# Kernel optimization log

Hardware: AMD Instinct MI355X
Metric: run time of the kernel (lower is better)

The kernel has to match this reference:

```python
import jax, jax.numpy as jnp
import numpy as np

N, E = 50000, 800000
DIN, DOUT, DEDGE, HEADS = 128, 128, 64, 1


def setup_inputs() -> dict:
    key = jax.random.key(0)
    ks = jax.random.split(key, 16)
    s = 0.02
    inp = {
        "x": jax.random.normal(ks[0], (N, DIN), jnp.float32),
        "edge_index": jax.random.randint(ks[1], (2, E), 0, N, dtype=jnp.int32),
        "edge_attr": jax.random.normal(ks[2], (E, DEDGE), jnp.float32),
        # TransformerConv params (PyG defaults: q/k/v/skip have bias, lin_edge has no bias)
        "Wq": jax.random.normal(ks[3], (DIN, HEADS * DOUT), jnp.float32) * s,
        "bq": jnp.zeros((HEADS * DOUT,), jnp.float32),
        "Wk": jax.random.normal(ks[4], (DIN, HEADS * DOUT), jnp.float32) * s,
        "bk": jnp.zeros((HEADS * DOUT,), jnp.float32),
        "Wv": jax.random.normal(ks[5], (DIN, HEADS * DOUT), jnp.float32) * s,
        "bv": jnp.zeros((HEADS * DOUT,), jnp.float32),
        "We": jax.random.normal(ks[6], (DEDGE, HEADS * DOUT), jnp.float32) * s,
        "Wskip": jax.random.normal(ks[7], (DIN, HEADS * DOUT), jnp.float32) * s,
        "bskip": jnp.zeros((HEADS * DOUT,), jnp.float32),
        # LayerNorm
        "ln_g": jnp.ones((DOUT,), jnp.float32),
        "ln_b": jnp.zeros((DOUT,), jnp.float32),
        # GatedResidualConnection
        "Wres": jax.random.normal(ks[8], (DIN, DOUT), jnp.float32) * s,
        "bres": jnp.zeros((DOUT,), jnp.float32),
        "Wgate": jax.random.normal(ks[9], (DIN, 1), jnp.float32) * s,
        "bgate": jnp.zeros((1,), jnp.float32),
    }
    return inp


def _transformer_conv(x, edge_index, edge_attr, Wq, bq, Wk, bk, Wv, bv, We, Wskip, bskip):
    H, C = HEADS, DOUT
    src, dst = edge_index[0], edge_index[1]  # j -> i (aggregate at dst)
    q = (x @ Wq + bq).reshape(-1, H, C)
    k = (x @ Wk + bk).reshape(-1, H, C)
    v = (x @ Wv + bv).reshape(-1, H, C)
    e = (edge_attr @ We).reshape(-1, H, C)  # [E,H,C]
    k_j = k[src] + e
    v_j = v[src] + e
    q_i = q[dst]
    alpha = jnp.sum(q_i * k_j, axis=-1) / jnp.sqrt(jnp.float32(C))  # [E,H]
    # segment softmax over incoming edges of each dst node
    amax = jax.ops.segment_max(alpha, dst, num_segments=N)  # [N,H]
    ex = jnp.exp(alpha - amax[dst])
    denom = jax.ops.segment_sum(ex, dst, num_segments=N)  # [N,H]
    p = ex / denom[dst]  # [E,H]
    out = jax.ops.segment_sum(p[..., None] * v_j, dst, num_segments=N)  # [N,H,C]
    out = out.reshape(-1, H * C)
    out = out + (x @ Wskip + bskip)  # root weight skip
    return out


def reference(x, edge_index, edge_attr, Wq, bq, Wk, bk, Wv, bv, We, Wskip, bskip,
              ln_g, ln_b, Wres, bres, Wgate, bgate):
    out = _transformer_conv(x, edge_index, edge_attr, Wq, bq, Wk, bk, Wv, bv, We, Wskip, bskip)
    # LayerNorm(out_channels)
    mu = jnp.mean(out, axis=-1, keepdims=True)
    var = jnp.mean(jnp.square(out - mu), axis=-1, keepdims=True)
    out = (out - mu) / jnp.sqrt(var + 1e-5) * ln_g + ln_b
    out = jax.nn.relu(out)
    # gated residual
    residual = x @ Wres + bres
    gate = jax.nn.sigmoid(x @ Wgate + bgate)  # [N,1]
    return gate * out + (1.0 - gate) * residual
```

## Files before the change

kernel.cpp:

```cpp
#include <hip/hip_runtime.h>
#include <math.h>

#define NN 50000
#define EE 800000
#define NPAD 50048
#define PC 768

typedef short bf16x8 __attribute__((ext_vector_type(8)));
typedef float f32x4 __attribute__((ext_vector_type(4)));

#define ASCALE 0.08838834764831845f

__device__ inline unsigned short f2bf(float f)
{
    unsigned u = __float_as_uint(f);
    u = u + 0x7fff + ((u >> 16) & 1);
    return (unsigned short)(u >> 16);
}

__device__ inline float bfu(unsigned short us)
{
    return __uint_as_float((unsigned)us << 16);
}

__global__ __launch_bounds__(256) void k_wprep(const float* __restrict__ Wq,
                                               const float* __restrict__ bq,
                                               const float* __restrict__ We,
                                               float* __restrict__ wqe,
                                               float* __restrict__ bqe)
{
    int idx = blockIdx.x * 256 + threadIdx.x;
    if (idx < 8192) {
        int r = idx >> 6, m = idx & 63;
        float acc = 0.f;
        for (int c = 0; c < 128; ++c) acc += Wq[r * 128 + c] * We[m * 128 + c];
        wqe[r * 64 + m] = acc;
    } else if (idx < 8256) {
        int m = idx - 8192;
        float acc = 0.f;
        for (int c = 0; c < 128; ++c) acc += bq[c] * We[m * 128 + c];
        bqe[m] = acc;
    }
}

__global__ __launch_bounds__(256) void k_packx(const float* __restrict__ x,
                                               short* __restrict__ Xb)
{
    int t = blockIdx.x * 256 + threadIdx.x;
    int base = t * 4;
    if (base >= NPAD * 128) return;
    short s0 = 0, s1 = 0, s2 = 0, s3 = 0;
    if (base < NN * 128) {
        const float4 v = *(const float4*)(x + base);
        s0 = f2bf(v.x); s1 = f2bf(v.y); s2 = f2bf(v.z); s3 = f2bf(v.w);
    }
    short4 o; o.x = s0; o.y = s1; o.z = s2; o.w = s3;
    *(short4*)(Xb + base) = o;
}

__global__ __launch_bounds__(256) void k_packw(
    const float* __restrict__ Wq, const float* __restrict__ bq,
    const float* __restrict__ Wk, const float* __restrict__ bk,
    const float* __restrict__ Wv, const float* __restrict__ bv,
    const float* __restrict__ Wskip, const float* __restrict__ bskip,
    const float* __restrict__ Wres, const float* __restrict__ bres,
    const float* __restrict__ Wgate, const float* __restrict__ bgate,
    const float* __restrict__ wqe, const float* __restrict__ bqe,
    const float* __restrict__ We,
    short* __restrict__ WT, float* __restrict__ bias,
    unsigned short* __restrict__ WeTb)
{
    int idx = blockIdx.x * 256 + threadIdx.x;
    if (idx < PC * 128) {
        int col = idx >> 7, k = idx & 127;
        float v;
        if (col < 128)      v = Wq[k * 128 + col];
        else if (col < 256) v = Wk[k * 128 + (col - 128)];
        else if (col < 384) v = Wv[k * 128 + (col - 256)];
        else if (col < 512) v = Wskip[k * 128 + (col - 384)];
        else if (col < 640) v = Wres[k * 128 + (col - 512)];
        else if (col < 704) v = wqe[k * 64 + (col - 640)];
        else if (col == 704) v = Wgate[k];
        else                v = 0.f;
        WT[col * 128 + k] = (short)f2bf(v);
    } else if (idx < PC * 128 + PC) {
        int col = idx - PC * 128;
        float b;
        if (col < 128)      b = bq[col];
        else if (col < 256) b = bk[col - 128];
        else if (col < 384) b = bv[col - 256];
        else if (col < 512) b = bskip[col - 384];
        else if (col < 640) b = bres[col - 512];
        else if (col < 704) b = bqe[col - 640];
        else if (col == 704) b = bgate[0];
        else                b = 0.f;
        bias[col] = b;
    } else if (idx < PC * 128 + PC + 128 * 72) {
        int i2 = idx - (PC * 128 + PC);
        int c = i2 / 72, kk = i2 % 72;
        WeTb[i2] = (kk < 64) ? f2bf(We[kk * 128 + c]) : (unsigned short)0;
    }
}

#define LROW 136
__global__ __launch_bounds__(256) void k_gemm(const short* __restrict__ Xb,
                                              const short* __restrict__ WT,
                                              const float* __restrict__ bias,
                                              float* __restrict__ Pq,
                                              unsigned short* __restrict__ Pe,
                                              unsigned short* __restrict__ KVb16)
{
    __shared__ short Al[128 * LROW];
    __shared__ short Bl[64 * LROW];

    int bn = blockIdx.x;
    int bm = blockIdx.y;
    int tid = threadIdx.x;

    const short* gA = Xb + (size_t)bm * 128 * 128;
    const short* gB = WT + (size_t)bn * 64 * 128;

#pragma unroll
    for (int it = 0; it < 8; ++it) {
        int g = it * 256 + tid;
        int row = g >> 4, c8 = g & 15;
        *(bf16x8*)&Al[row * LROW + c8 * 8] = *(const bf16x8*)(gA + g * 8);
    }
#pragma unroll
    for (int it = 0; it < 4; ++it) {
        int g = it * 256 + tid;
        int row = g >> 4, c8 = g & 15;
        *(bf16x8*)&Bl[row * LROW + c8 * 8] = *(const bf16x8*)(gB + g * 8);
    }
    __syncthreads();

    int wave = tid >> 6, lane = tid & 63;
    int quad = lane >> 4, l16 = lane & 15;
    int r0 = wave * 32;

    f32x4 acc[2][4] = {};
#pragma unroll
    for (int ks = 0; ks < 4; ++ks) {
        int k0 = ks * 32 + quad * 8;
        bf16x8 af0 = *(const bf16x8*)&Al[(r0 + l16) * LROW + k0];
        bf16x8 af1 = *(const bf16x8*)&Al[(r0 + 16 + l16) * LROW + k0];
#pragma unroll
        for (int cn = 0; cn < 4; ++cn) {
            bf16x8 bfr = *(const bf16x8*)&Bl[(cn * 16 + l16) * LROW + k0];
            acc[0][cn] = __builtin_amdgcn_mfma_f32_16x16x32_bf16(af0, bfr, acc[0][cn], 0, 0, 0);
            acc[1][cn] = __builtin_amdgcn_mfma_f32_16x16x32_bf16(af1, bfr, acc[1][cn], 0, 0, 0);
        }
    }

    bool isKV = (bn >= 2 && bn <= 5);
#pragma unroll
    for (int half = 0; half < 2; ++half) {
        int growb = bm * 128 + r0 + half * 16 + quad * 4;
#pragma unroll
        for (int cn = 0; cn < 4; ++cn) {
            int gcol = bn * 64 + cn * 16 + l16;
            float b = bias[gcol];
#pragma unroll
            for (int i = 0; i < 4; ++i) {
                int grow = growb + i;
                if (grow < NN) {
                    float v = acc[half][cn][i] + b;
                    if (bn < 2) {
                        Pq[(size_t)grow * 128 + gcol] = v;
                    } else if (isKV) {
                        int c, sub;
                        if (gcol < 192)      { c = gcol - 128; sub = 0; }
                        else if (gcol < 256) { c = gcol - 192; sub = 1; }
                        else if (gcol < 320) { c = gcol - 256; sub = 2; }
                        else                 { c = gcol - 320; sub = 3; }
                        KVb16[(size_t)grow * 256 + c * 4 + sub] = f2bf(v);
                    } else if (gcol <= 704) {
                        if (gcol == 704) v = 1.f / (1.f + __expf(-v));
                        Pe[(size_t)grow * 384 + (gcol - 384)] = f2bf(v);
                    }
                }
            }
        }
    }
}

__global__ __launch_bounds__(256) void k_hist(const int* __restrict__ ei,
                                              int* __restrict__ deg, int E)
{
    int e = blockIdx.x * 256 + threadIdx.x;
    if (e < E) atomicAdd(&deg[ei[E + e]], 1);
}

__global__ __launch_bounds__(256) void k_scan1(const int* __restrict__ deg,
                                               int* __restrict__ rs,
                                               int* __restrict__ cs, int n)
{
    __shared__ int sh[256];
    int base = blockIdx.x * 1024;
    int t = threadIdx.x;
    int idx = base + t * 4;
    int v[4];
#pragma unroll
    for (int k = 0; k < 4; ++k) v[k] = (idx + k < n) ? deg[idx + k] : 0;
    int sum = v[0] + v[1] + v[2] + v[3];
    sh[t] = sum;
    __syncthreads();
    for (int off = 1; off < 256; off <<= 1) {
        int add = (t >= off) ? sh[t - off] : 0;
        __syncthreads();
        sh[t] += add;
        __syncthreads();
    }
    int run = sh[t] - sum;
    if (t == 255) cs[blockIdx.x] = sh[255];
#pragma unroll
    for (int k = 0; k < 4; ++k) {
        if (idx + k < n) rs[idx + k] = run;
        run += v[k];
    }
}

__global__ void k_scan2(int* __restrict__ cs, int nc)
{
    __shared__ int sh[64];
    int t = threadIdx.x;
    sh[t] = (t < nc) ? cs[t] : 0;
    __syncthreads();
    if (t == 0) {
        int acc = 0;
        for (int i = 0; i < nc; ++i) { int v = sh[i]; sh[i] = acc; acc += v; }
    }
    __syncthreads();
    if (t < nc) cs[t] = sh[t];
}

__global__ __launch_bounds__(256) void k_scan3(int* __restrict__ rs,
                                               const int* __restrict__ cs,
                                               int* __restrict__ cur, int n, int E)
{
    int i = blockIdx.x * 256 + threadIdx.x;
    if (i < n) {
        int v = rs[i] + cs[i >> 10];
        rs[i] = v;
        cur[i] = v;
    } else if (i == n) {
        rs[n] = E;
    }
}

__global__ __launch_bounds__(256) void k_scatter(const int* __restrict__ ei,
                                                 int* __restrict__ cur,
                                                 int2* __restrict__ sj, int E)
{
    int e = blockIdx.x * 256 + threadIdx.x;
    if (e < E) {
        int d = ei[E + e];
        int pos = atomicAdd(&cur[d], 1);
        int2 v; v.x = ei[e]; v.y = e;
        sj[pos] = v;
    }
}

__global__ __launch_bounds__(256) void k_attn_fused(
    const float* __restrict__ Pq, const unsigned short* __restrict__ Pe,
    const unsigned int* __restrict__ KVb,
    const float* __restrict__ ea, const unsigned short* __restrict__ WeTb,
    const int* __restrict__ rs, const int2* __restrict__ sj,
    const float* __restrict__ ln_g, const float* __restrict__ ln_b,
    float* __restrict__ out)
{
    __shared__ unsigned short Sb_l[4 * 64];
    __shared__ float att_l[4 * 128];

    int tid = threadIdx.x;
    int wave = tid >> 6, lane = tid & 63;
    int node = blockIdx.x * 4 + wave;

    const float* Qrow = Pq + (size_t)node * 128;
    const unsigned short* Erow = Pe + (size_t)node * 384;
    float q0 = Qrow[lane];
    float q1 = Qrow[64 + lane];
    float wq = bfu(Erow[256 + lane]);

    float accd = 0.f, t0 = 0.f, t1 = 0.f, sA = 0.f;
    int beg = rs[node], end = rs[node + 1];

    int p = beg;
    for (; p + 8 <= end; p += 8) {
        float pp[8], aa[8], v0[8], v1[8];
#pragma unroll
        for (int u = 0; u < 8; ++u) {
            long long sv = __builtin_nontemporal_load((const long long*)(sj + p + u));
            int sx = (int)sv, sy = (int)(sv >> 32);
            uint2 kv2 = *(const uint2*)(KVb + (size_t)sx * 128 + 2 * lane);
            float a = __builtin_nontemporal_load(ea + (size_t)sy * 64 + lane);
            float k0 = __uint_as_float(kv2.x << 16);
            float k1 = __uint_as_float(kv2.x & 0xffff0000u);
            v0[u] = __uint_as_float(kv2.y << 16);
            v1[u] = __uint_as_float(kv2.y & 0xffff0000u);
            aa[u] = a;
            pp[u] = q0 * k0 + q1 * k1 + wq * a;
        }
#pragma unroll
        for (int o = 32; o > 0; o >>= 1) {
#pragma unroll
            for (int u = 0; u < 8; ++u) pp[u] += __shfl_xor(pp[u], o);
        }
#pragma unroll
        for (int u = 0; u < 8; ++u) {
            float ex = __expf(pp[u] * ASCALE);
            accd += ex;
            t0 += ex * v0[u];
            t1 += ex * v1[u];
            sA += ex * aa[u];
        }
    }
    for (; p + 4 <= end; p += 4) {
        float pp[4], aa[4], v0[4], v1[4];
#pragma unroll
        for (int u = 0; u < 4; ++u) {
            long long sv = __builtin_nontemporal_load((const long long*)(sj + p + u));
            int sx = (int)sv, sy = (int)(sv >> 32);
            uint2 kv2 = *(const uint2*)(KVb + (size_t)sx * 128 + 2 * lane);
            float a = __builtin_nontemporal_load(ea + (size_t)sy * 64 + lane);
            float k0 = __uint_as_float(kv2.x << 16);
            float k1 = __uint_as_float(kv2.x & 0xffff0000u);
            v0[u] = __uint_as_float(kv2.y << 16);
            v1[u] = __uint_as_float(kv2.y & 0xffff0000u);
            aa[u] = a;
            pp[u] = q0 * k0 + q1 * k1 + wq * a;
        }
#pragma unroll
        for (int o = 32; o > 0; o >>= 1) {
#pragma unroll
            for (int u = 0; u < 4; ++u) pp[u] += __shfl_xor(pp[u], o);
        }
#pragma unroll
        for (int u = 0; u < 4; ++u) {
            float ex = __expf(pp[u] * ASCALE);
            accd += ex;
            t0 += ex * v0[u];
            t1 += ex * v1[u];
            sA += ex * aa[u];
        }
    }
    for (; p < end; ++p) {
        long long sv = __builtin_nontemporal_load((const long long*)(sj + p));
        int sx = (int)sv, sy = (int)(sv >> 32);
        uint2 kv2 = *(const uint2*)(KVb + (size_t)sx * 128 + 2 * lane);
        float a = __builtin_nontemporal_load(ea + (size_t)sy * 64 + lane);
        float k0 = __uint_as_float(kv2.x << 16);
        float k1 = __uint_as_float(kv2.x & 0xffff0000u);
        float vv0 = __uint_as_float(kv2.y << 16);
        float vv1 = __uint_as_float(kv2.y & 0xffff0000u);
        float part = q0 * k0 + q1 * k1 + wq * a;
#pragma unroll
        for (int o = 32; o > 0; o >>= 1) part += __shfl_xor(part, o);
        float ex = __expf(part * ASCALE);
        accd += ex;
        t0 += ex * vv0;
        t1 += ex * vv1;
        sA += ex * a;
    }


    Sb_l[wave * 64 + lane] = f2bf(sA);
    {
        int quad = lane >> 4, l16 = lane & 15;
        bf16x8 a0 = *(const bf16x8*)&Sb_l[wave * 64 + quad * 8];
        bf16x8 a1 = *(const bf16x8*)&Sb_l[wave * 64 + 32 + quad * 8];
#pragma unroll
        for (int cn = 0; cn < 8; ++cn) {
            int r = cn * 16 + l16;
            bf16x8 b0 = *(const bf16x8*)(WeTb + r * 72 + quad * 8);
            bf16x8 b1 = *(const bf16x8*)(WeTb + r * 72 + 32 + quad * 8);
            f32x4 acc = {};
            acc = __builtin_amdgcn_mfma_f32_16x16x32_bf16(a0, b0, acc, 0, 0, 0);
            acc = __builtin_amdgcn_mfma_f32_16x16x32_bf16(a1, b1, acc, 0, 0, 0);
            if (quad == 0) att_l[wave * 128 + cn * 16 + l16] = acc[0];
        }
    }

    float rcp = accd > 0.f ? 1.f / accd : 0.f;
    float a0f = (t0 + att_l[wave * 128 + lane]) * rcp + bfu(Erow[lane]);
    float a1f = (t1 + att_l[wave * 128 + 64 + lane]) * rcp + bfu(Erow[64 + lane]);

    float s = a0f + a1f;
#pragma unroll
    for (int o = 32; o > 0; o >>= 1) s += __shfl_xor(s, o);
    float mean = s * (1.f / 128.f);
    float d0 = a0f - mean, d1 = a1f - mean;
    float vs = d0 * d0 + d1 * d1;
#pragma unroll
    for (int o = 32; o > 0; o >>= 1) vs += __shfl_xor(vs, o);
    float inv = rsqrtf(vs * (1.f / 128.f) + 1e-5f);
    float n0 = d0 * inv * ln_g[lane] + ln_b[lane];
    float n1 = d1 * inv * ln_g[64 + lane] + ln_b[64 + lane];
    n0 = fmaxf(n0, 0.f);
    n1 = fmaxf(n1, 0.f);

    float g = bfu(Erow[320]);
    float r0 = bfu(Erow[128 + lane]);
    float r1 = bfu(Erow[192 + lane]);
    out[(size_t)node * 128 + lane] = g * n0 + (1.f - g) * r0;
    out[(size_t)node * 128 + 64 + lane] = g * n1 + (1.f - g) * r1;
}

extern "C" void kernel_launch(void* const* d_in, const int* in_sizes, int n_in,
                              void* d_out, int out_size, void* d_ws, size_t ws_size,
                              hipStream_t stream)
{
    const float* x     = (const float*)d_in[0];
    const int*   ei    = (const int*)d_in[1];
    const float* ea    = (const float*)d_in[2];
    const float* Wq    = (const float*)d_in[3];
    const float* bq    = (const float*)d_in[4];
    const float* Wk    = (const float*)d_in[5];
    const float* bk    = (const float*)d_in[6];
    const float* Wv    = (const float*)d_in[7];
    const float* bv    = (const float*)d_in[8];
    const float* We    = (const float*)d_in[9];
    const float* Wskip = (const float*)d_in[10];
    const float* bskip = (const float*)d_in[11];
    const float* ln_g  = (const float*)d_in[12];
    const float* ln_b  = (const float*)d_in[13];
    const float* Wres  = (const float*)d_in[14];
    const float* bres  = (const float*)d_in[15];
    const float* Wgate = (const float*)d_in[16];
    const float* bgate = (const float*)d_in[17];
    float* out = (float*)d_out;

    float* W = (float*)d_ws;
    size_t o = 0;
    auto falloc = [&](size_t e) { size_t r = o; o += e; return r; };
    size_t oPQ   = falloc((size_t)NN * 128);
    size_t oWQE  = falloc(8192);
    size_t oBQE  = falloc(64);
    size_t oBIAS = falloc(PC);
    size_t oKVB  = falloc((size_t)NN * 128);

    short* SB = (short*)(W + o);
    size_t oXB  = 0;
    size_t oWT  = oXB + (size_t)NPAD * 128;
    size_t oWET = oWT + (size_t)PC * 128;
    size_t oPE  = oWET + 128 * 72;
    size_t sh_total = oPE + (size_t)NN * 384;

    int* IB = (int*)(SB + ((sh_total + 1) & ~(size_t)1));
    size_t io = 0;
    auto ialloc = [&](size_t e) { size_t r = io; io += e; return r; };
    size_t oSJ   = ialloc((size_t)2 * EE);
    size_t oDEG  = ialloc(NN);
    size_t oRS   = ialloc(NN + 1);
    size_t oCUR  = ialloc(NN);
    size_t oCS   = ialloc(64);

    hipMemsetAsync(IB + oDEG, 0, NN * sizeof(int), stream);

    k_wprep<<<33, 256, 0, stream>>>(Wq, bq, We, W + oWQE, W + oBQE);
    k_packx<<<(NPAD * 128 / 4 + 255) / 256, 256, 0, stream>>>(x, SB + oXB);
    k_packw<<<(PC * 128 + PC + 128 * 72 + 255) / 256, 256, 0, stream>>>(
        Wq, bq, Wk, bk, Wv, bv, Wskip, bskip, Wres, bres, Wgate, bgate,
        W + oWQE, W + oBQE, We, SB + oWT, W + oBIAS,
        (unsigned short*)(SB + oWET));

    dim3 ggrid(PC / 64, NPAD / 128);
    k_gemm<<<ggrid, 256, 0, stream>>>(SB + oXB, SB + oWT, W + oBIAS, W + oPQ,
                                      (unsigned short*)(SB + oPE),
                                      (unsigned short*)(W + oKVB));

    k_hist<<<(EE + 255) / 256, 256, 0, stream>>>(ei, IB + oDEG, EE);
    k_scan1<<<49, 256, 0, stream>>>(IB + oDEG, IB + oRS, IB + oCS, NN);
    k_scan2<<<1, 64, 0, stream>>>(IB + oCS, 49);
    k_scan3<<<(NN + 256) / 256, 256, 0, stream>>>(IB + oRS, IB + oCS, IB + oCUR, NN, EE);
    k_scatter<<<(EE + 255) / 256, 256, 0, stream>>>(ei, IB + oCUR, (int2*)(IB + oSJ), EE);

    k_attn_fused<<<NN / 4, 256, 0, stream>>>(
        W + oPQ, (const unsigned short*)(SB + oPE),
        (const unsigned int*)(W + oKVB), ea,
        (const unsigned short*)(SB + oWET),
        IB + oRS, (const int2*)(IB + oSJ), ln_g, ln_b, out);
}
```

Before: 596.8 us.

## Software-pipeline edge gathers and share the edge-attr MFMA across block waves

The main 8-edge loop now issues the gathers for the next batch of K/V rows and edge attributes before computing the current batch, so memory latency overlaps with the dot-product, shuffle and exp work. The per-wave projection of the summed edge attributes through We is restructured: all four waves' sums go into the MFMA A operand together and each wave computes two of the eight column tiles, then writes the results to shared memory for the others. This cuts redundant MFMA and weight loads per wave. The cost is two block-wide barriers and higher register pressure from the prefetch buffers, which may reduce occupancy.

New measurement: 619.6 us. +3.8%, slower.

```diff
diff --git a/kernel.cpp b/kernel.cpp
--- a/kernel.cpp
+++ b/kernel.cpp
@@ -285,21 +285,37 @@
     float accd = 0.f, t0 = 0.f, t1 = 0.f, sA = 0.f;
     int beg = rs[node], end = rs[node + 1];
 
+    int nb = (end - beg) >> 3;
     int p = beg;
-    for (; p + 8 <= end; p += 8) {
-        float pp[8], aa[8], v0[8], v1[8];
+
+    uint2 kv[8]; float av[8];
+    if (nb > 0) {
 #pragma unroll
         for (int u = 0; u < 8; ++u) {
             long long sv = __builtin_nontemporal_load((const long long*)(sj + p + u));
             int sx = (int)sv, sy = (int)(sv >> 32);
-            uint2 kv2 = *(const uint2*)(KVb + (size_t)sx * 128 + 2 * lane);
-            float a = __builtin_nontemporal_load(ea + (size_t)sy * 64 + lane);
-            float k0 = __uint_as_float(kv2.x << 16);
-            float k1 = __uint_as_float(kv2.x & 0xffff0000u);
-            v0[u] = __uint_as_float(kv2.y << 16);
-            v1[u] = __uint_as_float(kv2.y & 0xffff0000u);
-            aa[u] = a;
-            pp[u] = q0 * k0 + q1 * k1 + wq * a;
+            kv[u] = *(const uint2*)(KVb + (size_t)sx * 128 + 2 * lane);
+            av[u] = __builtin_nontemporal_load(ea + (size_t)sy * 64 + lane);
+        }
+    }
+    for (int b = 0; b < nb; ++b) {
+        uint2 kvn[8]; float avn[8];
+        int np = p + 8;
+        if (b + 1 < nb) {
+#pragma unroll
+            for (int u = 0; u < 8; ++u) {
+                long long sv = __builtin_nontemporal_load((const long long*)(sj + np + u));
+                int sx = (int)sv, sy = (int)(sv >> 32);
+                kvn[u] = *(const uint2*)(KVb + (size_t)sx * 128 + 2 * lane);
+                avn[u] = __builtin_nontemporal_load(ea + (size_t)sy * 64 + lane);
+            }
+        }
+        float pp[8];
+#pragma unroll
+        for (int u = 0; u < 8; ++u) {
+            float k0 = __uint_as_float(kv[u].x << 16);
+            float k1 = __uint_as_float(kv[u].x & 0xffff0000u);
+            pp[u] = q0 * k0 + q1 * k1 + wq * av[u];
         }
 #pragma unroll
         for (int o = 32; o > 0; o >>= 1) {
@@ -310,10 +326,15 @@
         for (int u = 0; u < 8; ++u) {
             float ex = __expf(pp[u] * ASCALE);
             accd += ex;
-            t0 += ex * v0[u];
-            t1 += ex * v1[u];
-            sA += ex * aa[u];
-        }
+            t0 += ex * __uint_as_float(kv[u].y << 16);
+            t1 += ex * __uint_as_float(kv[u].y & 0xffff0000u);
+            sA += ex * av[u];
+        }
+        if (b + 1 < nb) {
+#pragma unroll
+            for (int u = 0; u < 8; ++u) { kv[u] = kvn[u]; av[u] = avn[u]; }
+        }
+        p = np;
     }
     for (; p + 4 <= end; p += 4) {
         float pp[4], aa[4], v0[4], v1[4];
@@ -365,21 +386,30 @@
 
 
     Sb_l[wave * 64 + lane] = f2bf(sA);
+    __syncthreads();
+
     {
         int quad = lane >> 4, l16 = lane & 15;
-        bf16x8 a0 = *(const bf16x8*)&Sb_l[wave * 64 + quad * 8];
-        bf16x8 a1 = *(const bf16x8*)&Sb_l[wave * 64 + 32 + quad * 8];
-#pragma unroll
-        for (int cn = 0; cn < 8; ++cn) {
+        int arow = l16 & 3;
+        bf16x8 a0 = *(const bf16x8*)&Sb_l[arow * 64 + quad * 8];
+        bf16x8 a1 = *(const bf16x8*)&Sb_l[arow * 64 + 32 + quad * 8];
+#pragma unroll
+        for (int c2 = 0; c2 < 2; ++c2) {
+            int cn = wave * 2 + c2;
             int r = cn * 16 + l16;
             bf16x8 b0 = *(const bf16x8*)(WeTb + r * 72 + quad * 8);
             bf16x8 b1 = *(const bf16x8*)(WeTb + r * 72 + 32 + quad * 8);
             f32x4 acc = {};
             acc = __builtin_amdgcn_mfma_f32_16x16x32_bf16(a0, b0, acc, 0, 0, 0);
             acc = __builtin_amdgcn_mfma_f32_16x16x32_bf16(a1, b1, acc, 0, 0, 0);
-            if (quad == 0) att_l[wave * 128 + cn * 16 + l16] = acc[0];
-        }
-    }
+            if (quad == 0) {
+#pragma unroll
+                for (int i = 0; i < 4; ++i)
+                    att_l[i * 128 + cn * 16 + l16] = acc[i];
+            }
+        }
+    }
+    __syncthreads();
 
     float rcp = accd > 0.f ? 1.f / accd : 0.f;
     float a0f = (t0 + att_l[wave * 128 + lane]) * rcp + bfu(Erow[lane]);
```
